# Kernel optimization log

Hardware: AMD Instinct MI355X
Metric: run time of the kernel (lower is better)

## Reference

```python
import jax, jax.numpy as jnp
from jax import lax
import numpy as np

DIM, HEADS, WIN = 192, 8, 8
B, H, W = 4, 256, 256


def setup_inputs() -> dict:
    key = jax.random.key(0)
    ks = jax.random.split(key, 4)
    s = 0.02
    return {
        "x": jax.random.normal(ks[0], (B, DIM, H, W), jnp.float32),
        "temperature": jnp.ones((HEADS, 1, 1), jnp.float32),
        "qkv_w": jax.random.normal(ks[1], (3 * DIM, DIM, 1, 1), jnp.float32) * s,
        "qkv_b": jnp.zeros((3 * DIM,), jnp.float32),
        "dw_w": jax.random.normal(ks[2], (3 * DIM, 1, 3, 3), jnp.float32) * s,
        "dw_b": jnp.zeros((3 * DIM,), jnp.float32),
        "proj_w": jax.random.normal(ks[3], (DIM, DIM, 1, 1), jnp.float32) * s,
        "proj_b": jnp.zeros((DIM,), jnp.float32),
    }


def _conv(x, w, b, groups=1, pad='VALID'):
    y = lax.conv_general_dilated(x, w, (1, 1), pad,
                                 feature_group_count=groups,
                                 dimension_numbers=('NCHW', 'OIHW', 'NCHW'))
    return y + b[None, :, None, None]


def _l2norm(x, eps=1e-12):
    # F.normalize(dim=-1): x / max(||x||_2, eps)
    n = jnp.sqrt(jnp.sum(x * x, axis=-1, keepdims=True))
    return x / jnp.maximum(n, eps)


def _chan_attn(q, k, v, temp):
    # q,k,v: [n, heads, c_per_head, d]; channel-wise (CxC) attention
    q = _l2norm(q)
    k = _l2norm(k)
    attn = jnp.einsum('nhcd,nhed->nhce', q, k) * temp[None]
    attn = jax.nn.softmax(attn, axis=-1)
    return jnp.einsum('nhce,nhed->nhcd', attn, v)


def reference(x, temperature, qkv_w, qkv_b, dw_w, dw_b, proj_w, proj_b):
    b, c, h, w = x.shape
    win, heads = WIN, HEADS
    cph = c // heads

    qkv = _conv(x, qkv_w, qkv_b)
    qkv = _conv(qkv, dw_w, dw_b, groups=3 * c, pad='SAME')  # depthwise 3x3
    q, k, v = jnp.split(qkv, 3, axis=1)

    # ---- local (windowed) branch ----
    def win_part(t):
        t = t.reshape(b, c, h // win, win, w // win, win)
        t = t.transpose(0, 2, 4, 1, 3, 5)
        return t.reshape(-1, heads, cph, win * win)

    o1 = _chan_attn(win_part(q), win_part(k), win_part(v), temperature)
    o1 = o1.reshape(b, h // win, w // win, c, win, win)
    o1 = o1.transpose(0, 3, 1, 4, 2, 5).reshape(b, c, h, w)

    # ---- global branch ----
    def flat(t):
        return t.reshape(b, heads, cph, h * w)

    o2 = _chan_attn(flat(q), flat(k), flat(v), temperature)
    o2 = o2.reshape(b, c, h, w)

    return _conv(o1 + o2, proj_w, proj_b)
```

## Files before the change

### kernel.cpp

```cpp
#include <hip/hip_runtime.h>
#include <hip/hip_bf16.h>
#include <cstdint>
#include <cstddef>

#define HWPIX 65536
#define IMGW 256
#define CDIM 192
#define C3 576
#define NBATCH 4
#define NHEADS 8
#define CPH 24
#define KP 104

using bf16 = __hip_bfloat16;
typedef __attribute__((ext_vector_type(8))) short short8;
typedef __attribute__((ext_vector_type(4))) float f32x4;
typedef unsigned int u32;
typedef unsigned short u16;

__device__ __forceinline__ float b2f(bf16 v) { return __bfloat162float(v); }
__device__ __forceinline__ bf16 f2b(float v) { return __float2bfloat16(v); }
__device__ __forceinline__ float bu2f(u16 h) { return __uint_as_float((u32)h << 16); }
__device__ __forceinline__ u16 f2bu(float x) {
    bf16 h = __float2bfloat16(x);
    return *reinterpret_cast<u16*>(&h);
}
__device__ __forceinline__ u32 pack2(float a, float b) {
    return (u32)f2bu(a) | ((u32)f2bu(b) << 16);
}

__global__ __launch_bounds__(256) void prep_weights(
    const float* __restrict__ W, u16* __restrict__ Wb, int n)
{
    int i = blockIdx.x * 256 + threadIdx.x;
    if (i < n) Wb[i] = f2bu(W[i]);
}

__global__ __launch_bounds__(256) void xprep_kernel(
    const float* __restrict__ X, u16* __restrict__ Xt)
{
    __shared__ float sX[CDIM * 68];
    const int b  = blockIdx.y;
    const int p0 = blockIdx.x * 64;
    const int tid = threadIdx.x;

#pragma unroll
    for (int i = 0; i < 12; ++i) {
        const int idx = tid + i * 256;
        const int p4 = idx & 15, k = idx >> 4;
        const float4 v = *reinterpret_cast<const float4*>(
            X + ((size_t)b * CDIM + k) * HWPIX + p0 + p4 * 4);
        *reinterpret_cast<float4*>(&sX[k * 68 + p4 * 4]) = v;
    }
    __syncthreads();

    const int p = tid >> 2;
    const int seg = tid & 3;
    u16* dst = Xt + ((size_t)b * HWPIX + p0 + p) * CDIM;
#pragma unroll
    for (int s = 0; s < 6; ++s) {
        const int blk = seg * 6 + s;
        float f[8];
#pragma unroll
        for (int j = 0; j < 8; ++j) f[j] = sX[(blk * 8 + j) * 68 + p];
        uint4 ov;
        ov.x = pack2(f[0], f[1]);
        ov.y = pack2(f[2], f[3]);
        ov.z = pack2(f[4], f[5]);
        ov.w = pack2(f[6], f[7]);
        *reinterpret_cast<uint4*>(dst + blk * 8) = ov;
    }
}

__global__ __launch_bounds__(256, 4) void conv_qkv_mfma(
    const u16* __restrict__ Xt, const u16* __restrict__ Wb,
    const float* __restrict__ bias, bf16* __restrict__ Y)
{
    __shared__ alignas(16) u16 sA[64 * KP];
    __shared__ alignas(16) u16 sB[128 * KP];
    __shared__ float sBias[64];

    int lin = blockIdx.x;
    lin = (lin & 7) * (18432 / 8) + (lin >> 3);
    const int co_t = lin % 9;
    const int rest = lin / 9;
    const int p_t = rest & 511;
    const int b   = rest >> 9;
    const int co0 = co_t * 64;
    const int p0  = p_t * 128;

    const int tid  = threadIdx.x;
    const int wave = tid >> 6;
    const int lane = tid & 63;
    const int r  = lane & 15;
    const int hk = lane >> 4;

    if (tid < 64) sBias[tid] = bias[co0 + tid];

    f32x4 acc[4][2];
#pragma unroll
    for (int i = 0; i < 4; ++i)
#pragma unroll
        for (int j = 0; j < 2; ++j) acc[i][j] = (f32x4){0.f, 0.f, 0.f, 0.f};

#pragma unroll
    for (int c = 0; c < 2; ++c) {
        {
            int idx = tid;
#pragma unroll
            for (int i = 0; i < 3; ++i, idx += 256) {
                const int row = idx / 12, cv = idx % 12;
                const uint4 v = *reinterpret_cast<const uint4*>(
                    Wb + (size_t)(co0 + row) * CDIM + c * 96 + cv * 8);
                *reinterpret_cast<uint4*>(&sA[row * KP + cv * 8]) = v;
            }
        }
        {
            int idx = tid;
#pragma unroll
            for (int i = 0; i < 6; ++i, idx += 256) {
                const int row = idx / 12, cv = idx % 12;
                const uint4 v = *reinterpret_cast<const uint4*>(
                    Xt + ((size_t)b * HWPIX + p0 + row) * CDIM + c * 96 + cv * 8);
                *reinterpret_cast<uint4*>(&sB[row * KP + cv * 8]) = v;
            }
        }
        __syncthreads();

#pragma unroll
        for (int ks = 0; ks < 3; ++ks) {
            const int kof = ks * 32 + hk * 8;
            const u16* pA = &sA[r * KP + kof];
            const u16* pB = &sB[(wave * 32 + r) * KP + kof];
            const short8 a0 = *reinterpret_cast<const short8*>(pA);
            const short8 a1 = *reinterpret_cast<const short8*>(pA + 16 * KP);
            const short8 a2 = *reinterpret_cast<const short8*>(pA + 32 * KP);
            const short8 a3 = *reinterpret_cast<const short8*>(pA + 48 * KP);
            const short8 b0 = *reinterpret_cast<const short8*>(pB);
            const short8 b1 = *reinterpret_cast<const short8*>(pB + 16 * KP);
            acc[0][0] = __builtin_amdgcn_mfma_f32_16x16x32_bf16(a0, b0, acc[0][0], 0, 0, 0);
            acc[1][0] = __builtin_amdgcn_mfma_f32_16x16x32_bf16(a1, b0, acc[1][0], 0, 0, 0);
            acc[2][0] = __builtin_amdgcn_mfma_f32_16x16x32_bf16(a2, b0, acc[2][0], 0, 0, 0);
            acc[3][0] = __builtin_amdgcn_mfma_f32_16x16x32_bf16(a3, b0, acc[3][0], 0, 0, 0);
            acc[0][1] = __builtin_amdgcn_mfma_f32_16x16x32_bf16(a0, b1, acc[0][1], 0, 0, 0);
            acc[1][1] = __builtin_amdgcn_mfma_f32_16x16x32_bf16(a1, b1, acc[1][1], 0, 0, 0);
            acc[2][1] = __builtin_amdgcn_mfma_f32_16x16x32_bf16(a2, b1, acc[2][1], 0, 0, 0);
            acc[3][1] = __builtin_amdgcn_mfma_f32_16x16x32_bf16(a3, b1, acc[3][1], 0, 0, 0);
        }
        __syncthreads();
    }

    u16* sOut = sB;
#pragma unroll
    for (int mf = 0; mf < 4; ++mf) {
#pragma unroll
        for (int j = 0; j < 4; ++j) {
            const int row = mf * 16 + hk * 4 + j;
            const float bs = sBias[row];
            sOut[row * 128 + wave * 32 + r]      = f2bu(acc[mf][0][j] + bs);
            sOut[row * 128 + wave * 32 + r + 16] = f2bu(acc[mf][1][j] + bs);
        }
    }
    __syncthreads();
#pragma unroll
    for (int i = 0; i < 4; ++i) {
        const int idx = tid + i * 256;
        const int row = idx >> 4, cq = idx & 15;
        const uint4 v = *reinterpret_cast<const uint4*>(&sOut[row * 128 + cq * 8]);
        *reinterpret_cast<uint4*>(
            &Y[((size_t)b * C3 + co0 + row) * HWPIX + p0 + cq * 8]) = v;
    }
}

__global__ __launch_bounds__(256, 4) void conv_proj_mfma(
    const float* __restrict__ X, const u16* __restrict__ Wb,
    const float* __restrict__ bias, float* __restrict__ Y)
{
    __shared__ alignas(16) u16 sA[64 * KP];
    __shared__ alignas(16) u16 sB[128 * KP];
    __shared__ float sBias[64];

    int lin = blockIdx.x;
    lin = (lin & 7) * (6144 / 8) + (lin >> 3);
    const int co_t = lin % 3;
    const int rest = lin / 3;
    const int p_t = rest & 511;
    const int b   = rest >> 9;
    const int co0 = co_t * 64;
    const int p0  = p_t * 128;

    const int tid  = threadIdx.x;
    const int wave = tid >> 6;
    const int lane = tid & 63;
    const int r  = lane & 15;
    const int hk = lane >> 4;

    if (tid < 64) sBias[tid] = bias[co0 + tid];

    f32x4 acc[4][2];
#pragma unroll
    for (int i = 0; i < 4; ++i)
#pragma unroll
        for (int j = 0; j < 2; ++j) acc[i][j] = (f32x4){0.f, 0.f, 0.f, 0.f};

    const int kp_lane = tid & 7;
    const int p4      = tid >> 3;

#pragma unroll
    for (int c = 0; c < 2; ++c) {
        {
            int idx = tid;
#pragma unroll
            for (int i = 0; i < 3; ++i, idx += 256) {
                const int row = idx / 12, cv = idx % 12;
                const uint4 v = *reinterpret_cast<const uint4*>(
                    Wb + (size_t)(co0 + row) * CDIM + c * 96 + cv * 8);
                *reinterpret_cast<uint4*>(&sA[row * KP + cv * 8]) = v;
            }
        }
        {
            const float* Xc = X + ((size_t)b * CDIM + c * 96) * HWPIX + p0;
#pragma unroll
            for (int i = 0; i < 6; ++i) {
                const int kp = kp_lane + i * 8;
                const int k  = kp * 2;
                const float4 va = *reinterpret_cast<const float4*>(
                    Xc + (size_t)k * HWPIX + p4 * 4);
                const float4 vb = *reinterpret_cast<const float4*>(
                    Xc + (size_t)(k + 1) * HWPIX + p4 * 4);
                const int col = (((k >> 3) ^ (p4 & 3)) << 3) | (k & 7);
                const float av[4] = {va.x, va.y, va.z, va.w};
                const float bv[4] = {vb.x, vb.y, vb.z, vb.w};
#pragma unroll
                for (int j = 0; j < 4; ++j) {
                    const int row = p4 * 4 + j;
                    *reinterpret_cast<u32*>(&sB[row * KP + col]) = pack2(av[j], bv[j]);
                }
            }
        }
        __syncthreads();

#pragma unroll
        for (int ks = 0; ks < 3; ++ks) {
            const int kof = ks * 32 + hk * 8;
            const u16* pA = &sA[r * KP + kof];
            const int rowb = wave * 32 + r;
            const int colr = (((kof >> 3) ^ ((rowb >> 2) & 3)) << 3);
            const u16* pB = &sB[rowb * KP + colr];
            const short8 a0 = *reinterpret_cast<const short8*>(pA);
            const short8 a1 = *reinterpret_cast<const short8*>(pA + 16 * KP);
            const short8 a2 = *reinterpret_cast<const short8*>(pA + 32 * KP);
            const short8 a3 = *reinterpret_cast<const short8*>(pA + 48 * KP);
            const short8 b0 = *reinterpret_cast<const short8*>(pB);
            const short8 b1 = *reinterpret_cast<const short8*>(pB + 16 * KP);
            acc[0][0] = __builtin_amdgcn_mfma_f32_16x16x32_bf16(a0, b0, acc[0][0], 0, 0, 0);
            acc[1][0] = __builtin_amdgcn_mfma_f32_16x16x32_bf16(a1, b0, acc[1][0], 0, 0, 0);
            acc[2][0] = __builtin_amdgcn_mfma_f32_16x16x32_bf16(a2, b0, acc[2][0], 0, 0, 0);
            acc[3][0] = __builtin_amdgcn_mfma_f32_16x16x32_bf16(a3, b0, acc[3][0], 0, 0, 0);
            acc[0][1] = __builtin_amdgcn_mfma_f32_16x16x32_bf16(a0, b1, acc[0][1], 0, 0, 0);
            acc[1][1] = __builtin_amdgcn_mfma_f32_16x16x32_bf16(a1, b1, acc[1][1], 0, 0, 0);
            acc[2][1] = __builtin_amdgcn_mfma_f32_16x16x32_bf16(a2, b1, acc[2][1], 0, 0, 0);
            acc[3][1] = __builtin_amdgcn_mfma_f32_16x16x32_bf16(a3, b1, acc[3][1], 0, 0, 0);
        }
        __syncthreads();
    }

#pragma unroll
    for (int mf = 0; mf < 4; ++mf) {
#pragma unroll
        for (int j = 0; j < 4; ++j) {
            const int co = co0 + mf * 16 + hk * 4 + j;
            const float bs = sBias[mf * 16 + hk * 4 + j];
            const size_t base = ((size_t)b * CDIM + co) * HWPIX + p0 + wave * 32 + r;
            Y[base]      = acc[mf][0][j] + bs;
            Y[base + 16] = acc[mf][1][j] + bs;
        }
    }
}

__global__ __launch_bounds__(256) void dwconv_kernel(
    const bf16* __restrict__ In, const float* __restrict__ Wd,
    const float* __restrict__ bd, bf16* __restrict__ Out)
{
    __shared__ alignas(16) u16 sIn[10 * 256];
    const int bc = blockIdx.y;
    const int c = bc % C3;
    const size_t base = (size_t)bc * HWPIX;
    const int r0 = blockIdx.x * 8;
    const int tid = threadIdx.x;

    for (int idx = tid; idx < 320; idx += 256) {
        const int lr = idx >> 5, ch = idx & 31;
        const int gr = r0 + lr - 1;
        uint4 v = {0u, 0u, 0u, 0u};
        if ((unsigned)gr < IMGW)
            v = *reinterpret_cast<const uint4*>(&In[base + (size_t)gr * IMGW + ch * 8]);
        *reinterpret_cast<uint4*>(&sIn[lr * 256 + ch * 8]) = v;
    }
    __syncthreads();

    float wg[9];
#pragma unroll
    for (int t = 0; t < 9; ++t) wg[t] = Wd[c * 9 + t];

    const int rr = tid >> 5;
    const int px0 = (tid & 31) * 8;
    const float bias = bd[c];
    float acc[8];
#pragma unroll
    for (int j = 0; j < 8; ++j) acc[j] = bias;

#pragma unroll
    for (int dy = 0; dy < 3; ++dy) {
        const int row = rr + dy;
        const u16* rp = &sIn[row * 256];
        const short8 mv = *reinterpret_cast<const short8*>(&rp[px0]);
        float m[8];
#pragma unroll
        for (int j = 0; j < 8; ++j) m[j] = bu2f((u16)mv[j]);
        const float lft = (px0 > 0) ? bu2f(rp[px0 - 1]) : 0.f;
        const float rgt = (px0 + 8 < 256) ? bu2f(rp[px0 + 8]) : 0.f;
        const float w0 = wg[dy * 3], w1 = wg[dy * 3 + 1], w2 = wg[dy * 3 + 2];

        acc[0] = fmaf(w0, lft, acc[0]);
        acc[0] = fmaf(w1, m[0], acc[0]);
        acc[0] = fmaf(w2, m[1], acc[0]);
#pragma unroll
        for (int j = 1; j < 7; ++j) {
            acc[j] = fmaf(w0, m[j - 1], acc[j]);
            acc[j] = fmaf(w1, m[j], acc[j]);
            acc[j] = fmaf(w2, m[j + 1], acc[j]);
        }
        acc[7] = fmaf(w0, m[6], acc[7]);
        acc[7] = fmaf(w1, m[7], acc[7]);
        acc[7] = fmaf(w2, rgt, acc[7]);
    }

    uint4 ov;
    ov.x = pack2(acc[0], acc[1]);
    ov.y = pack2(acc[2], acc[3]);
    ov.z = pack2(acc[4], acc[5]);
    ov.w = pack2(acc[6], acc[7]);
    *reinterpret_cast<uint4*>(&Out[base + (size_t)(r0 + rr) * IMGW + px0]) = ov;
}

#define CS 328
#define PS 40

__global__ __launch_bounds__(256) void local_attn_kernel(
    const bf16* __restrict__ QKV, const float* __restrict__ temp,
    const float* __restrict__ Ag, float* __restrict__ Osum)
{
    __shared__ alignas(16) u16 sQ[32 * CS];
    __shared__ alignas(16) u16 sK[32 * CS];
    __shared__ alignas(16) u16 sV[32 * CS];
    __shared__ alignas(16) u16 sP[4 * 32 * PS];
    __shared__ float snq[4 * 32], snk[4 * 32];
    __shared__ float sAg[576];

    const int wy    = blockIdx.x >> 3;
    const int strip = blockIdx.x & 7;
    const int head  = blockIdx.y;
    const int b     = blockIdx.z;
    const int x0    = strip * 32;
    const int tid   = threadIdx.x;
    const int w     = tid >> 6;
    const int lane  = tid & 63;
    const int r     = lane & 15;
    const int hk    = lane >> 4;

    {
        const float* Asrc = Ag + ((size_t)(b * NHEADS + head)) * 576;
        for (int idx = tid; idx < 576; idx += 256) sAg[idx] = Asrc[idx];
    }

#pragma unroll
    for (int i = 0; i < 9; ++i) {
        const int idx = tid + i * 256;
        const int tensor = idx / 768;
        const int rem = idx - tensor * 768;
        const int c  = rem >> 5;
        const int rw = (rem >> 2) & 7;
        const int ch = rem & 3;
        const size_t g = ((size_t)b * C3 + tensor * CDIM + head * CPH + c) * HWPIX
                       + (size_t)(wy * 8 + rw) * IMGW + x0 + ch * 8;
        const uint4 v = *reinterpret_cast<const uint4*>(&QKV[g]);
        u16* dst = (tensor == 0) ? sQ : ((tensor == 1) ? sK : sV);
        *reinterpret_cast<uint4*>(&dst[c * CS + rw * 40 + ch * 8]) = v;
    }
    __syncthreads();

    if (tid < 192) {
        const int qk = tid / 96;
        const int rem = tid - qk * 96;
        const int ww = rem / 24, c = rem % 24;
        const u16* sT = qk ? sK : sQ;
        const int off = c * CS + ww * 8;
        float s = 0.f;
#pragma unroll
        for (int rw = 0; rw < 8; ++rw) {
            const short8 v = *reinterpret_cast<const short8*>(&sT[off + rw * 40]);
#pragma unroll
            for (int j = 0; j < 8; ++j) {
                const float f = bu2f((u16)v[j]);
                s = fmaf(f, f, s);
            }
        }
        const float inv = 1.f / fmaxf(sqrtf(s), 1e-12f);
        if (qk) snk[ww * 32 + c] = inv; else snq[ww * 32 + c] = inv;
    }
    __syncthreads();

    f32x4 accg[2][2];
#pragma unroll
    for (int i = 0; i < 2; ++i)
#pragma unroll
        for (int j = 0; j < 2; ++j) accg[i][j] = (f32x4){0.f, 0.f, 0.f, 0.f};

#pragma unroll
    for (int kk = 0; kk < 2; ++kk) {
        const int colA = (kk * 4 + hk) * 40 + w * 8;
        const short8 aq0 = *reinterpret_cast<const short8*>(&sQ[(r     ) * CS + colA]);
        const short8 aq1 = *reinterpret_cast<const short8*>(&sQ[(16 + r) * CS + colA]);
        const short8 bk0 = *reinterpret_cast<const short8*>(&sK[(r     ) * CS + colA]);
        const short8 bk1 = *reinterpret_cast<const short8*>(&sK[(16 + r) * CS + colA]);
        accg[0][0] = __builtin_amdgcn_mfma_f32_16x16x32_bf16(aq0, bk0, accg[0][0], 0, 0, 0);
        accg[0][1] = __builtin_amdgcn_mfma_f32_16x16x32_bf16(aq0, bk1, accg[0][1], 0, 0, 0);
        accg[1][0] = __builtin_amdgcn_mfma_f32_16x16x32_bf16(aq1, bk0, accg[1][0], 0, 0, 0);
        accg[1][1] = __builtin_amdgcn_mfma_f32_16x16x32_bf16(aq1, bk1, accg[1][1], 0, 0, 0);
    }

    const float t = temp[head];
    const int e0 = lane & 15;
    const bool v1 = e0 < 8;
    const float ink0 = snk[w * 32 + e0];
    const float ink1 = snk[w * 32 + 16 + e0];

#pragma unroll
    for (int ct = 0; ct < 2; ++ct) {
#pragma unroll
        for (int j = 0; j < 4; ++j) {
            const int cidx = ct * 16 + hk * 4 + j;
            const float inq = snq[w * 32 + cidx];
            const float g0 = accg[ct][0][j] * inq * ink0 * t;
            const float g1 = v1 ? accg[ct][1][j] * inq * ink1 * t : -1e30f;
            float m = fmaxf(g0, g1);
#pragma unroll
            for (int mk = 8; mk >= 1; mk >>= 1) m = fmaxf(m, __shfl_xor(m, mk));
            const float p0 = __expf(g0 - m);
            const float p1 = v1 ? __expf(g1 - m) : 0.f;
            float s = p0 + p1;
#pragma unroll
            for (int mk = 8; mk >= 1; mk >>= 1) s += __shfl_xor(s, mk);
            const float inv = 1.f / s;
            if (cidx < CPH) {
                sP[w * 32 * PS + cidx * PS + e0] = f2bu(p0 * inv + sAg[cidx * CPH + e0]);
                if (v1) sP[w * 32 * PS + cidx * PS + 16 + e0]
                    = f2bu(p1 * inv + sAg[cidx * CPH + 16 + e0]);
            }
        }
    }
    __syncthreads();

    f32x4 acco[2][4];
#pragma unroll
    for (int i = 0; i < 2; ++i)
#pragma unroll
        for (int j = 0; j < 4; ++j) acco[i][j] = (f32x4){0.f, 0.f, 0.f, 0.f};

    short8 afr[2];
#pragma unroll
    for (int ct = 0; ct < 2; ++ct) {
        if (hk < 3)
            afr[ct] = *reinterpret_cast<const short8*>(
                &sP[w * 32 * PS + (ct * 16 + r) * PS + hk * 8]);
        else
            afr[ct] = (short8){0, 0, 0, 0, 0, 0, 0, 0};
    }
#pragma unroll
    for (int nt = 0; nt < 4; ++nt) {
        const int px = nt * 16 + r;
        const int colV = (px >> 3) * 40 + w * 8 + (px & 7);
        short8 bfr;
        if (hk < 3) {
#pragma unroll
            for (int j = 0; j < 8; ++j)
                bfr[j] = (short)sV[(hk * 8 + j) * CS + colV];
        } else {
            bfr = (short8){0, 0, 0, 0, 0, 0, 0, 0};
        }
        acco[0][nt] = __builtin_amdgcn_mfma_f32_16x16x32_bf16(afr[0], bfr, acco[0][nt], 0, 0, 0);
        acco[1][nt] = __builtin_amdgcn_mfma_f32_16x16x32_bf16(afr[1], bfr, acco[1][nt], 0, 0, 0);
    }

    const size_t ob = ((size_t)b * CDIM + head * CPH) * HWPIX;
#pragma unroll
    for (int ct = 0; ct < 2; ++ct) {
#pragma unroll
        for (int j = 0; j < 4; ++j) {
            const int cidx = ct * 16 + hk * 4 + j;
            if (cidx >= CPH) continue;
#pragma unroll
            for (int nt = 0; nt < 4; ++nt) {
                const int px = nt * 16 + r;
                const int rpx = px >> 3, pxl = px & 7;
                Osum[ob + (size_t)cidx * HWPIX
                     + (size_t)(wy * 8 + rpx) * IMGW + x0 + w * 8 + pxl] = acco[ct][nt][j];
            }
        }
    }
}

#define GRS 520

__global__ __launch_bounds__(256) void gstats_kernel(
    const bf16* __restrict__ QKV, float* __restrict__ Gp)
{
    __shared__ alignas(16) u16 sq[32 * GRS];
    __shared__ alignas(16) u16 sk[32 * GRS];

    const int chunk = blockIdx.x;
    const int bh = blockIdx.y;
    const int b = bh >> 3, head = bh & 7;
    const int tid = threadIdx.x;
    const int w = tid >> 6, lane = tid & 63;
    const int r = lane & 15, hk = lane >> 4;

    const size_t qb = ((size_t)b * C3 + head * CPH) * HWPIX;
    const size_t kb = qb + (size_t)CDIM * HWPIX;

    for (int idx = tid; idx < 1040; idx += 256) {
        const int t = idx >= 520;
        const int o = idx - t * 520;
        u16* d = (t ? sk : sq) + 24 * GRS + o * 8;
        *reinterpret_cast<uint4*>(d) = (uint4){0u, 0u, 0u, 0u};
    }

    f32x4 acc[2][2];
#pragma unroll
    for (int i = 0; i < 2; ++i)
#pragma unroll
        for (int j = 0; j < 2; ++j) acc[i][j] = (f32x4){0.f, 0.f, 0.f, 0.f};
    float nacc = 0.f;
    const int nrow = tid >> 2;
    const int nq4  = tid & 3;

    for (int st = 0; st < 8; ++st) {
        const int d0 = chunk * 4096 + st * 512;
        __syncthreads();
#pragma unroll
        for (int i = 0; i < 12; ++i) {
            const int idx = tid + i * 256;
            const int t = idx >= 1536;
            const int rem = idx - t * 1536;
            const int c = rem >> 6, dv = rem & 63;
            const uint4 v = *reinterpret_cast<const uint4*>(
                &QKV[(t ? kb : qb) + (size_t)c * HWPIX + d0 + dv * 8]);
            u16* dst = (t ? sk : sq) + c * GRS + dv * 8;
            *reinterpret_cast<uint4*>(dst) = v;
        }
        __syncthreads();

#pragma unroll
        for (int ks = 0; ks < 4; ++ks) {
            const int kof = w * 128 + ks * 32 + hk * 8;
            const short8 aq0 = *reinterpret_cast<const short8*>(&sq[(r     ) * GRS + kof]);
            const short8 aq1 = *reinterpret_cast<const short8*>(&sq[(16 + r) * GRS + kof]);
            const short8 bk0 = *reinterpret_cast<const short8*>(&sk[(r     ) * GRS + kof]);
            const short8 bk1 = *reinterpret_cast<const short8*>(&sk[(16 + r) * GRS + kof]);
            acc[0][0] = __builtin_amdgcn_mfma_f32_16x16x32_bf16(aq0, bk0, acc[0][0], 0, 0, 0);
            acc[0][1] = __builtin_amdgcn_mfma_f32_16x16x32_bf16(aq0, bk1, acc[0][1], 0, 0, 0);
            acc[1][0] = __builtin_amdgcn_mfma_f32_16x16x32_bf16(aq1, bk0, acc[1][0], 0, 0, 0);
            acc[1][1] = __builtin_amdgcn_mfma_f32_16x16x32_bf16(aq1, bk1, acc[1][1], 0, 0, 0);
        }

        if (nrow < 48) {
            const u16* rp = (nrow < 24 ? &sq[nrow * GRS] : &sk[(nrow - 24) * GRS]) + nq4 * 128;
#pragma unroll
            for (int i = 0; i < 16; ++i) {
                const short8 v = *reinterpret_cast<const short8*>(&rp[i * 8]);
#pragma unroll
                for (int j = 0; j < 8; ++j) {
                    const float f = bu2f((u16)v[j]);
                    nacc = fmaf(f, f, nacc);
                }
            }
        }
    }
    __syncthreads();

    float* red = reinterpret_cast<float*>(sq);
#pragma unroll
    for (int ct = 0; ct < 2; ++ct) {
#pragma unroll
        for (int et = 0; et < 2; ++et) {
#pragma unroll
            for (int j = 0; j < 4; ++j) {
                const int c = ct * 16 + hk * 4 + j;
                const int e = et * 16 + r;
                if (c < CPH && e < CPH)
                    red[(w * 24 + c) * 25 + e] = acc[ct][et][j];
            }
        }
    }
    __syncthreads();

    float* dst = Gp + ((size_t)bh * 32 + chunk) * 624;
    for (int idx = tid; idx < 576; idx += 256) {
        const int c = idx / 24, e = idx % 24;
        const int o = c * 25 + e;
        dst[idx] = red[o] + red[600 + o] + red[1200 + o] + red[1800 + o];
    }

    float ns = nacc;
    ns += __shfl_xor(ns, 1);
    ns += __shfl_xor(ns, 2);
    if (nrow < 48 && nq4 == 0) {
        if (nrow < 24) dst[576 + nrow] = ns;
        else           dst[600 + (nrow - 24)] = ns;
    }
}

__global__ __launch_bounds__(64) void gsoftmax_kernel(
    const float* __restrict__ Gp, const float* __restrict__ temp,
    float* __restrict__ A)
{
    __shared__ float red[624];
    const int bh = blockIdx.x, head = bh & 7;
    const int tid = threadIdx.x;

    for (int jj = tid; jj < 624; jj += 64) {
        float s = 0.f;
        for (int ch = 0; ch < 16; ++ch) s += Gp[((size_t)bh * 32 + ch) * 624 + jj];
        red[jj] = s;
    }
    __syncthreads();

    if (tid < CPH) {
        const int c = tid;
        const float t = temp[head];
        const float inq = 1.f / fmaxf(sqrtf(red[576 + c]), 1e-12f);
        float l[CPH]; float m = -1e30f;
        for (int e = 0; e < CPH; ++e) {
            const float ink = 1.f / fmaxf(sqrtf(red[600 + e]), 1e-12f);
            l[e] = red[c * CPH + e] * inq * ink * t;
            m = fmaxf(m, l[e]);
        }
        float s = 0.f;
        for (int e = 0; e < CPH; ++e) { l[e] = expf(l[e] - m); s += l[e]; }
        const float inv = 1.f / s;
        for (int e = 0; e < CPH; ++e) A[(size_t)bh * 576 + c * CPH + e] = l[e] * inv;
    }
}

extern "C" void kernel_launch(void* const* d_in, const int* in_sizes, int n_in,
                              void* d_out, int out_size, void* d_ws, size_t ws_size,
                              hipStream_t stream) {
    const float* x           = (const float*)d_in[0];
    const float* temperature = (const float*)d_in[1];
    const float* qkv_w       = (const float*)d_in[2];
    const float* qkv_b       = (const float*)d_in[3];
    const float* dw_w        = (const float*)d_in[4];
    const float* dw_b        = (const float*)d_in[5];
    const float* proj_w      = (const float*)d_in[6];
    const float* proj_b      = (const float*)d_in[7];
    float* out = (float*)d_out;

    char* ws = (char*)d_ws;
    constexpr size_t QKV_ELEMS = (size_t)NBATCH * C3 * HWPIX;
    constexpr size_t QKV_BYTES = QKV_ELEMS * sizeof(bf16);

    bf16* qkv1 = (bf16*)ws;
    bf16* qkv2 = (bf16*)(ws + QKV_BYTES);
    float* osum = (float*)ws;
    float* Gp   = (float*)(ws + 2 * QKV_BYTES);
    float* Amat = Gp + (size_t)32 * 32 * 624;
    u16*  Wb    = (u16*)Gp;
    u16*  Wpb   = (u16*)(Amat + 32 * 576);
    u16*  Xt    = (u16*)qkv2;

    prep_weights<<<(C3 * CDIM + 255) / 256, 256, 0, stream>>>(qkv_w, Wb, C3 * CDIM);
    prep_weights<<<(CDIM * CDIM + 255) / 256, 256, 0, stream>>>(proj_w, Wpb, CDIM * CDIM);

    xprep_kernel<<<dim3(HWPIX / 64, NBATCH), 256, 0, stream>>>(x, Xt);

    conv_qkv_mfma<<<9 * 512 * NBATCH, 256, 0, stream>>>(Xt, Wb, qkv_b, qkv1);

    dwconv_kernel<<<dim3(32, NBATCH * C3), 256, 0, stream>>>(
        qkv1, dw_w, dw_b, qkv2);

    gstats_kernel<<<dim3(16, 32), 256, 0, stream>>>(qkv2, Gp);

    gsoftmax_kernel<<<32, 64, 0, stream>>>(Gp, temperature, Amat);

    local_attn_kernel<<<dim3(256, NHEADS, NBATCH), 256, 0, stream>>>(
        qkv2, temperature, Amat, osum);

    conv_proj_mfma<<<3 * 512 * NBATCH, 256, 0, stream>>>(osum, Wpb, proj_b, out);
}
```

Measured before the change: 679.1 us.

## Store local attention output as bf16 via LDS-staged coalesced writes

The local attention kernel now writes its output sum as bf16 rather than fp32. The output is staged through shared memory, which reuses the Q/K buffers, so the global stores become coalesced 16-byte writes. Shared memory is shrunk to 24-row Q/K/V buffers, the P and O tiles alias that space, and the launch bounds request 3 blocks per SM for higher occupancy. The projection conv now reads bf16 input, halving its load traffic, and the norm loop rotates its LDS rows to reduce bank conflicts. The cost is reduced precision in the intermediate sum and extra syncthreads barriers.

```diff
diff --git a/kernel.cpp b/kernel.cpp
--- a/kernel.cpp
+++ b/kernel.cpp
@@ -173,7 +173,7 @@
 }
 
 __global__ __launch_bounds__(256, 4) void conv_proj_mfma(
-    const float* __restrict__ X, const u16* __restrict__ Wb,
+    const u16* __restrict__ X, const u16* __restrict__ Wb,
     const float* __restrict__ bias, float* __restrict__ Y)
 {
     __shared__ alignas(16) u16 sA[64 * KP];
@@ -203,8 +203,8 @@
 #pragma unroll
         for (int j = 0; j < 2; ++j) acc[i][j] = (f32x4){0.f, 0.f, 0.f, 0.f};
 
-    const int kp_lane = tid & 7;
-    const int p4      = tid >> 3;
+    const int p4 = tid & 31;
+    const int kq = tid >> 5;
 
 #pragma unroll
     for (int c = 0; c < 2; ++c) {
@@ -219,23 +219,25 @@
             }
         }
         {
-            const float* Xc = X + ((size_t)b * CDIM + c * 96) * HWPIX + p0;
+            const u16* Xc = X + ((size_t)b * CDIM + c * 96) * HWPIX + p0;
 #pragma unroll
             for (int i = 0; i < 6; ++i) {
-                const int kp = kp_lane + i * 8;
+                const int kp = kq + i * 8;
                 const int k  = kp * 2;
-                const float4 va = *reinterpret_cast<const float4*>(
+                const uint2 va = *reinterpret_cast<const uint2*>(
                     Xc + (size_t)k * HWPIX + p4 * 4);
-                const float4 vb = *reinterpret_cast<const float4*>(
+                const uint2 vb = *reinterpret_cast<const uint2*>(
                     Xc + (size_t)(k + 1) * HWPIX + p4 * 4);
-                const int col = (((k >> 3) ^ (p4 & 3)) << 3) | (k & 7);
-                const float av[4] = {va.x, va.y, va.z, va.w};
-                const float bv[4] = {vb.x, vb.y, vb.z, vb.w};
-#pragma unroll
-                for (int j = 0; j < 4; ++j) {
-                    const int row = p4 * 4 + j;
-                    *reinterpret_cast<u32*>(&sB[row * KP + col]) = pack2(av[j], bv[j]);
-                }
+                const int col = (((kp >> 2) ^ (p4 & 3)) << 3) | (k & 7);
+                const u32 w0 = (va.x & 0xffffu) | (vb.x << 16);
+                const u32 w1 = (va.x >> 16)     | (vb.x & 0xffff0000u);
+                const u32 w2 = (va.y & 0xffffu) | (vb.y << 16);
+                const u32 w3 = (va.y >> 16)     | (vb.y & 0xffff0000u);
+                const int rb = p4 * 4;
+                *reinterpret_cast<u32*>(&sB[(rb    ) * KP + col]) = w0;
+                *reinterpret_cast<u32*>(&sB[(rb + 1) * KP + col]) = w1;
+                *reinterpret_cast<u32*>(&sB[(rb + 2) * KP + col]) = w2;
+                *reinterpret_cast<u32*>(&sB[(rb + 3) * KP + col]) = w3;
             }
         }
         __syncthreads();
@@ -346,17 +348,20 @@
 
 #define CS 328
 #define PS 40
-
-__global__ __launch_bounds__(256) void local_attn_kernel(
+#define OS 36
+
+__global__ __launch_bounds__(256, 3) void local_attn_kernel(
     const bf16* __restrict__ QKV, const float* __restrict__ temp,
-    const float* __restrict__ Ag, float* __restrict__ Osum)
+    const float* __restrict__ Ag, u16* __restrict__ Osum)
 {
-    __shared__ alignas(16) u16 sQ[32 * CS];
-    __shared__ alignas(16) u16 sK[32 * CS];
-    __shared__ alignas(16) u16 sV[32 * CS];
-    __shared__ alignas(16) u16 sP[4 * 32 * PS];
+    __shared__ alignas(16) u16 sMem[3 * 24 * CS];
     __shared__ float snq[4 * 32], snk[4 * 32];
     __shared__ float sAg[576];
+    u16* const sQ = sMem;
+    u16* const sK = sMem + 24 * CS;
+    u16* const sV = sMem + 48 * CS;
+    u16* const sP = sQ;
+    u16* const sO = sK;
 
     const int wy    = blockIdx.x >> 3;
     const int strip = blockIdx.x & 7;
@@ -385,7 +390,7 @@
         const size_t g = ((size_t)b * C3 + tensor * CDIM + head * CPH + c) * HWPIX
                        + (size_t)(wy * 8 + rw) * IMGW + x0 + ch * 8;
         const uint4 v = *reinterpret_cast<const uint4*>(&QKV[g]);
-        u16* dst = (tensor == 0) ? sQ : ((tensor == 1) ? sK : sV);
+        u16* dst = sMem + tensor * (24 * CS);
         *reinterpret_cast<uint4*>(&dst[c * CS + rw * 40 + ch * 8]) = v;
     }
     __syncthreads();
@@ -399,7 +404,8 @@
         float s = 0.f;
 #pragma unroll
         for (int rw = 0; rw < 8; ++rw) {
-            const short8 v = *reinterpret_cast<const short8*>(&sT[off + rw * 40]);
+            const int rw2 = (rw + c) & 7;
+            const short8 v = *reinterpret_cast<const short8*>(&sT[off + rw2 * 40]);
 #pragma unroll
             for (int j = 0; j < 8; ++j) {
                 const float f = bu2f((u16)v[j]);
@@ -429,6 +435,7 @@
         accg[1][0] = __builtin_amdgcn_mfma_f32_16x16x32_bf16(aq1, bk0, accg[1][0], 0, 0, 0);
         accg[1][1] = __builtin_amdgcn_mfma_f32_16x16x32_bf16(aq1, bk1, accg[1][1], 0, 0, 0);
     }
+    __syncthreads();
 
     const float t = temp[head];
     const int e0 = lane & 15;
@@ -441,7 +448,7 @@
 #pragma unroll
         for (int j = 0; j < 4; ++j) {
             const int cidx = ct * 16 + hk * 4 + j;
-            const float inq = snq[w * 32 + cidx];
+            const float inq = snq[w * 32 + (cidx < CPH ? cidx : 0)];
             const float g0 = accg[ct][0][j] * inq * ink0 * t;
             const float g1 = v1 ? accg[ct][1][j] * inq * ink1 * t : -1e30f;
             float m = fmaxf(g0, g1);
@@ -493,7 +500,6 @@
         acco[1][nt] = __builtin_amdgcn_mfma_f32_16x16x32_bf16(afr[1], bfr, acco[1][nt], 0, 0, 0);
     }
 
-    const size_t ob = ((size_t)b * CDIM + head * CPH) * HWPIX;
 #pragma unroll
     for (int ct = 0; ct < 2; ++ct) {
 #pragma unroll
@@ -504,10 +510,25 @@
             for (int nt = 0; nt < 4; ++nt) {
                 const int px = nt * 16 + r;
                 const int rpx = px >> 3, pxl = px & 7;
-                Osum[ob + (size_t)cidx * HWPIX
-                     + (size_t)(wy * 8 + rpx) * IMGW + x0 + w * 8 + pxl] = acco[ct][nt][j];
-            }
-        }
+                sO[(rpx * 24 + cidx) * OS + w * 8 + pxl] = f2bu(acco[ct][nt][j]);
+            }
+        }
+    }
+    __syncthreads();
+
+#pragma unroll
+    for (int i = 0; i < 3; ++i) {
+        const int idx = tid + i * 256;
+        const int q4 = idx & 3;
+        const int row = idx >> 2;
+        const int c = row % 24, rw = row / 24;
+        const u16* src = &sO[row * OS + q4 * 8];
+        const uint2 lo = *reinterpret_cast<const uint2*>(src);
+        const uint2 hi = *reinterpret_cast<const uint2*>(src + 4);
+        uint4 v = {lo.x, lo.y, hi.x, hi.y};
+        *reinterpret_cast<uint4*>(
+            &Osum[((size_t)b * CDIM + head * CPH + c) * HWPIX
+                  + (size_t)(wy * 8 + rw) * IMGW + x0 + q4 * 8]) = v;
     }
 }
 
@@ -672,7 +693,7 @@
 
     bf16* qkv1 = (bf16*)ws;
     bf16* qkv2 = (bf16*)(ws + QKV_BYTES);
-    float* osum = (float*)ws;
+    u16*  osum = (u16*)ws;
     float* Gp   = (float*)(ws + 2 * QKV_BYTES);
     float* Amat = Gp + (size_t)32 * 32 * 624;
     u16*  Wb    = (u16*)Gp;
```

Result: faster. 616.8 us (-9.2%).
